# Optimization experiments

Measured on AMD Instinct MI355X. Metric: run time of the kernel, lower is better.

## Reference

```python
import jax, jax.numpy as jnp
import numpy as np

N_FEATURES = 3072
LATENT_DIM = 128
BATCH = 8192


def setup_inputs() -> dict:
    key = jax.random.key(0)
    k1, k2, k3, k4 = jax.random.split(key, 4)
    example = jax.random.normal(k1, (BATCH, N_FEATURES), dtype=jnp.float32)
    # small-ish W so C = W W^T + sigma^2 I is well conditioned
    W = jax.random.normal(k2, (N_FEATURES, LATENT_DIM), dtype=jnp.float32) * 0.05
    log_var = jax.random.normal(k3, (1,), dtype=jnp.float32) * 0.1
    training_mean = jax.random.normal(k4, (N_FEATURES,), dtype=jnp.float32)
    return {"example": example, "W": W, "log_var": log_var, "training_mean": training_mean}


def reference(example, W, log_var, training_mean):
    n = W.shape[0]
    # C = W W^T + exp(log_var) * I   -- [n, n] covariance, as in the original
    C = W @ W.T + jnp.exp(log_var[0]) * jnp.eye(n, dtype=W.dtype)
    _, logdetC = jnp.linalg.slogdet(C)
    precision = jnp.linalg.inv(C)
    res = example.reshape(-1, n) - training_mean.reshape(1, n)  # [B, n]
    # diag(res @ precision @ res^T) computed directly, avoiding the BxB matrix
    quad = jnp.einsum("bi,ij,bj->b", res, precision, res)  # [B]
    log_2pi = np.log(2.0 * np.pi).astype(np.float32)
    log_like = -0.5 * (n * log_2pi + logdetC + quad)  # [B]
    return log_like
```

## Files before the change

kernel.cpp:

```cpp
#include <hip/hip_runtime.h>
#include <hip/hip_bf16.h>

#define N_FEAT 3072
#define LATENT 128
#define LOG2PI 1.8378770664093453f
#define GB 512
#define KHALF 1536

typedef __attribute__((ext_vector_type(8))) short short8;
typedef __attribute__((ext_vector_type(4))) float f32x4;

__device__ __forceinline__ unsigned short f2bf(float x) {
  unsigned int u = __float_as_uint(x);
  u += 0x7FFFu + ((u >> 16) & 1u);
  return (unsigned short)(u >> 16);
}

#define GR_CHUNK 64
__global__ __launch_bounds__(256) void k_prep(const float* __restrict__ W,
                                              float* __restrict__ M,
                                              unsigned short* __restrict__ Wt) {
  __shared__ __align__(16) float Ws[GR_CHUNK * 128];
  int t = threadIdx.x;
  int k0 = blockIdx.x * GR_CHUNK;
  const float* src = W + (size_t)k0 * 128;
#pragma unroll
  for (int c = 0; c < 8; ++c)
    ((float4*)Ws)[t + 256 * c] = ((const float4*)src)[t + 256 * c];
  __syncthreads();
  int tr = t >> 4, tc = t & 15;
  float acc[8][8];
#pragma unroll
  for (int r = 0; r < 8; ++r)
#pragma unroll
    for (int c = 0; c < 8; ++c) acc[r][c] = 0.f;
#pragma unroll 2
  for (int k = 0; k < GR_CHUNK; ++k) {
    f32x4 a0 = *(f32x4*)&Ws[k * 128 + 8 * tr];
    f32x4 a1 = *(f32x4*)&Ws[k * 128 + 8 * tr + 4];
    f32x4 b0 = *(f32x4*)&Ws[k * 128 + 8 * tc];
    f32x4 b1 = *(f32x4*)&Ws[k * 128 + 8 * tc + 4];
    float av[8] = {a0.x, a0.y, a0.z, a0.w, a1.x, a1.y, a1.z, a1.w};
    float bv[8] = {b0.x, b0.y, b0.z, b0.w, b1.x, b1.y, b1.z, b1.w};
#pragma unroll
    for (int r = 0; r < 8; ++r)
#pragma unroll
      for (int c = 0; c < 8; ++c) acc[r][c] = fmaf(av[r], bv[c], acc[r][c]);
  }
  float* dst = M + (size_t)(8 * tr) * 128 + 8 * tc;
#pragma unroll
  for (int r = 0; r < 8; ++r)
#pragma unroll
    for (int c = 0; c < 8; ++c) atomicAdd(&dst[r * 128 + c], acc[r][c]);
  int n = t >> 1, h = t & 1;
  unsigned pk[16];
#pragma unroll
  for (int c = 0; c < 16; ++c)
    pk[c] = (unsigned)f2bf(Ws[(h * 32 + 2 * c) * 128 + n]) |
            ((unsigned)f2bf(Ws[(h * 32 + 2 * c + 1) * 128 + n]) << 16);
  uint4* wd = (uint4*)(Wt + (size_t)n * N_FEAT + k0 + h * 32);
#pragma unroll
  for (int c = 0; c < 4; ++c)
    wd[c] = make_uint4(pk[4 * c], pk[4 * c + 1], pk[4 * c + 2], pk[4 * c + 3]);
}

__global__ __launch_bounds__(512, 4) void k_gemm(
    const float* __restrict__ ex, const float* __restrict__ mean,
    const unsigned short* __restrict__ Wt, float* __restrict__ M,
    float* __restrict__ scal, const float* __restrict__ log_var,
    float* __restrict__ T, float* __restrict__ sumsq) {
  __shared__ __align__(16) unsigned short As[2][32][72];
  __shared__ __align__(16) unsigned short Bs[2][128][72];
  __shared__ float prow[2][128], pcol[2][128], dbuf[2], diag[128], red[2];
  int t = threadIdx.x;

  if (blockIdx.x == GB) {
    bool act = t < 256;
    int itr = t >> 4, itc = t & 15;
    float lv = log_var[0];
    float sig2 = expf(lv);
    float a[8][8];
    if (act) {
      const float* srcM = M + (size_t)(8 * itr) * 128 + 8 * itc;
#pragma unroll
      for (int r = 0; r < 8; ++r) {
        f32x4 v0 = *(const f32x4*)(srcM + r * 128);
        f32x4 v1 = *(const f32x4*)(srcM + r * 128 + 4);
        a[r][0] = v0.x; a[r][1] = v0.y; a[r][2] = v0.z; a[r][3] = v0.w;
        a[r][4] = v1.x; a[r][5] = v1.y; a[r][6] = v1.z; a[r][7] = v1.w;
      }
      if (itr == itc) {
#pragma unroll
        for (int r = 0; r < 8; ++r) a[r][r] += sig2;
      }
      if (itr == 0) {
#pragma unroll
        for (int c = 0; c < 8; ++c) prow[0][8 * itc + c] = a[0][c];
      }
      if (itc == 0) {
#pragma unroll
        for (int r = 0; r < 8; ++r) pcol[0][8 * itr + r] = a[r][0];
      }
      if (t == 0) dbuf[0] = a[0][0];
    }
    __syncthreads();
    for (int kb = 0; kb < 16; ++kb) {
#pragma unroll
      for (int lk = 0; lk < 8; ++lk) {
        const int k = kb * 8 + lk;
        const int buf = k & 1;
        if (act) {
          float d = dbuf[buf];
          if (t == 0) diag[k] = d;
          float p = 1.0f / d;
          float pr[8], pc[8];
#pragma unroll
          for (int c = 0; c < 8; ++c) pr[c] = prow[buf][8 * itc + c] * p;
#pragma unroll
          for (int r = 0; r < 8; ++r) pc[r] = pcol[buf][8 * itr + r];
#pragma unroll
          for (int r = 0; r < 8; ++r)
#pragma unroll
            for (int c = 0; c < 8; ++c) a[r][c] = fmaf(-pc[r], pr[c], a[r][c]);
          bool myrow = (itr == (k >> 3));
          bool mycol = (itc == (k >> 3));
          if (myrow) {
#pragma unroll
            for (int c = 0; c < 8; ++c) a[lk][c] = pr[c];
          }
          if (mycol) {
#pragma unroll
            for (int r = 0; r < 8; ++r) a[r][lk] = -p * pc[r];
          }
          if (myrow && mycol) a[lk][lk] = p;
          if (k + 1 < 128) {
            const int nb = buf ^ 1;
            const int nl = (lk + 1) & 7;
            const int nr = (k + 1) >> 3;
            if (itr == nr) {
#pragma unroll
              for (int c = 0; c < 8; ++c) prow[nb][8 * itc + c] = a[nl][c];
            }
            if (itc == nr) {
#pragma unroll
              for (int r = 0; r < 8; ++r) pcol[nb][8 * itr + r] = a[r][nl];
            }
            if (itr == nr && itc == nr) dbuf[nb] = a[nl][nl];
          }
        }
        __syncthreads();
      }
    }
    if (act) {
      float* dst = M + (size_t)(8 * itr) * 128 + 8 * itc;
#pragma unroll
      for (int r = 0; r < 8; ++r) {
        f32x4 v0 = {a[r][0], a[r][1], a[r][2], a[r][3]};
        f32x4 v1 = {a[r][4], a[r][5], a[r][6], a[r][7]};
        *(f32x4*)(dst + r * 128) = v0;
        *(f32x4*)(dst + r * 128 + 4) = v1;
      }
    }
    float ld = 0.f;
    if (t < 128) ld = logf(diag[t]);
#pragma unroll
    for (int o = 1; o < 64; o <<= 1) ld += __shfl_xor(ld, o);
    if (t == 0) red[0] = ld;
    if (t == 64) red[1] = ld;
    __syncthreads();
    if (t == 0) {
      scal[0] = -0.5f * (N_FEAT * LOG2PI + (float)(N_FEAT - LATENT) * lv +
                         (red[0] + red[1]));
      scal[1] = expf(-lv);
    }
    return;
  }

  int half = blockIdx.x >> 8;
  int r0 = (blockIdx.x & 255) * 32;
  int kbase = half * KHALF;

  int arow = t >> 4, aseg = t & 15;
  const float* ep = ex + (size_t)(r0 + arow) * N_FEAT + kbase + aseg * 4;
  const float* mp = mean + kbase + aseg * 4;
  int sA = (((aseg >> 1) + arow) & 7) * 8 + (aseg & 1) * 4;
  int brow = t >> 2, bq = t & 3;
  const unsigned short* wp = Wt + (size_t)brow * N_FEAT + kbase + bq * 16;
  int sB = ((bq + brow) & 3) * 16;

  int lane = t & 63, w = t >> 6;
  int wr = w & 1, wc = w >> 1;
  int fr = lane & 15, fq = lane >> 4;
  int ar = wr * 16 + fr;
  int cA0 = ((fq + ar) & 7) * 8;
  int cA1 = ((fq + 4 + ar) & 7) * 8;
  int n0 = wc * 32 + fr, n1 = n0 + 16;
  int c00 = (((fq >> 1) + n0) & 3) * 16 + (fq & 1) * 8;
  int c01 = (((fq >> 1) + 2 + n0) & 3) * 16 + (fq & 1) * 8;
  int c10 = (((fq >> 1) + n1) & 3) * 16 + (fq & 1) * 8;
  int c11 = (((fq >> 1) + 2 + n1) & 3) * 16 + (fq & 1) * 8;

  f32x4 acc0 = {0.f, 0.f, 0.f, 0.f}, acc1 = {0.f, 0.f, 0.f, 0.f};
  float sq = 0.f;

  float4 e = *(const float4*)ep;
  float4 m = *(const float4*)mp;
  uint4 g0 = *(const uint4*)wp;
  uint4 g1 = *(const uint4*)(wp + 8);

#pragma unroll 2
  for (int it = 0; it < 24; ++it) {
    const int buf = it & 1;
    float rx = e.x - m.x, ry = e.y - m.y, rz = e.z - m.z, rw = e.w - m.w;
    sq = fmaf(rx, rx, sq); sq = fmaf(ry, ry, sq);
    sq = fmaf(rz, rz, sq); sq = fmaf(rw, rw, sq);
    uint2 pa;
    pa.x = (unsigned)f2bf(rx) | ((unsigned)f2bf(ry) << 16);
    pa.y = (unsigned)f2bf(rz) | ((unsigned)f2bf(rw) << 16);
    *(uint2*)&As[buf][arow][sA] = pa;
    *(uint4*)&Bs[buf][brow][sB] = g0;
    *(uint4*)&Bs[buf][brow][sB + 8] = g1;
    __syncthreads();
    if (it + 1 < 24) {
      e = *(const float4*)(ep + (it + 1) * 64);
      m = *(const float4*)(mp + (it + 1) * 64);
      g0 = *(const uint4*)(wp + (it + 1) * 64);
      g1 = *(const uint4*)(wp + (it + 1) * 64 + 8);
    }
    short8 a0 = *(const short8*)&As[buf][ar][cA0];
    short8 a1 = *(const short8*)&As[buf][ar][cA1];
    short8 b00 = *(const short8*)&Bs[buf][n0][c00];
    short8 b01 = *(const short8*)&Bs[buf][n0][c01];
    short8 b10 = *(const short8*)&Bs[buf][n1][c10];
    short8 b11 = *(const short8*)&Bs[buf][n1][c11];
    acc0 = __builtin_amdgcn_mfma_f32_16x16x32_bf16(a0, b00, acc0, 0, 0, 0);
    acc0 = __builtin_amdgcn_mfma_f32_16x16x32_bf16(a1, b01, acc0, 0, 0, 0);
    acc1 = __builtin_amdgcn_mfma_f32_16x16x32_bf16(a0, b10, acc1, 0, 0, 0);
    acc1 = __builtin_amdgcn_mfma_f32_16x16x32_bf16(a1, b11, acc1, 0, 0, 0);
  }

  sq += __shfl_xor(sq, 1); sq += __shfl_xor(sq, 2);
  sq += __shfl_xor(sq, 4); sq += __shfl_xor(sq, 8);
  if (aseg == 0) atomicAdd(&sumsq[r0 + arow], sq);

  float* tp = T + (size_t)(r0 + wr * 16 + fq * 4) * 128 + wc * 32 + fr;
#pragma unroll
  for (int ii = 0; ii < 4; ++ii) {
    atomicAdd(tp + (size_t)ii * 128, acc0[ii]);
    atomicAdd(tp + (size_t)ii * 128 + 16, acc1[ii]);
  }
}

__global__ __launch_bounds__(256) void k_epi(const float* __restrict__ T,
                                             const float* __restrict__ sumsq,
                                             const float* __restrict__ Minv,
                                             const float* __restrict__ scal,
                                             float* __restrict__ out) {
  __shared__ __align__(16) float Ts[32][132];
  __shared__ float rs[32];
  int t = threadIdx.x;
  int r0 = blockIdx.x * 32;
  int sr = t >> 3, sseg = t & 7;
  const float* tp = T + (size_t)(r0 + sr) * 128 + sseg * 16;
#pragma unroll
  for (int c = 0; c < 4; ++c) {
    float4 v = *(const float4*)(tp + c * 4);
    *(f32x4*)&Ts[sr][sseg * 16 + c * 4] = (f32x4){v.x, v.y, v.z, v.w};
  }
  if (t < 32) rs[t] = sumsq[r0 + t];
  __syncthreads();

  int rp = t >> 4, cg = t & 15;
  int ra = 2 * rp, rb = ra + 1;
  int c0 = cg * 8;
  float ya[8] = {0, 0, 0, 0, 0, 0, 0, 0};
  float yb[8] = {0, 0, 0, 0, 0, 0, 0, 0};
#pragma unroll 4
  for (int j = 0; j < 128; ++j) {
    float tav = Ts[ra][j];
    float tbv = Ts[rb][j];
    float4 v0 = *(const float4*)(Minv + j * LATENT + c0);
    float4 v1 = *(const float4*)(Minv + j * LATENT + c0 + 4);
    ya[0] = fmaf(tav, v0.x, ya[0]); ya[1] = fmaf(tav, v0.y, ya[1]);
    ya[2] = fmaf(tav, v0.z, ya[2]); ya[3] = fmaf(tav, v0.w, ya[3]);
    ya[4] = fmaf(tav, v1.x, ya[4]); ya[5] = fmaf(tav, v1.y, ya[5]);
    ya[6] = fmaf(tav, v1.z, ya[6]); ya[7] = fmaf(tav, v1.w, ya[7]);
    yb[0] = fmaf(tbv, v0.x, yb[0]); yb[1] = fmaf(tbv, v0.y, yb[1]);
    yb[2] = fmaf(tbv, v0.z, yb[2]); yb[3] = fmaf(tbv, v0.w, yb[3]);
    yb[4] = fmaf(tbv, v1.x, yb[4]); yb[5] = fmaf(tbv, v1.y, yb[5]);
    yb[6] = fmaf(tbv, v1.z, yb[6]); yb[7] = fmaf(tbv, v1.w, yb[7]);
  }
  float q0 = 0.f, q1 = 0.f;
#pragma unroll
  for (int c = 0; c < 8; ++c) {
    q0 = fmaf(ya[c], Ts[ra][c0 + c], q0);
    q1 = fmaf(yb[c], Ts[rb][c0 + c], q1);
  }
  q0 += __shfl_xor(q0, 1); q0 += __shfl_xor(q0, 2);
  q0 += __shfl_xor(q0, 4); q0 += __shfl_xor(q0, 8);
  q1 += __shfl_xor(q1, 1); q1 += __shfl_xor(q1, 2);
  q1 += __shfl_xor(q1, 4); q1 += __shfl_xor(q1, 8);
  if (cg == 0) {
    float cc = scal[0], is2 = scal[1];
    out[r0 + ra] = cc - 0.5f * is2 * (rs[ra] - q0);
    out[r0 + rb] = cc - 0.5f * is2 * (rs[rb] - q1);
  }
}

extern "C" void kernel_launch(void* const* d_in, const int* in_sizes, int n_in,
                              void* d_out, int out_size, void* d_ws, size_t ws_size,
                              hipStream_t stream) {
  (void)in_sizes; (void)n_in; (void)out_size; (void)ws_size;
  const float* ex   = (const float*)d_in[0];
  const float* W    = (const float*)d_in[1];
  const float* lv   = (const float*)d_in[2];
  const float* mean = (const float*)d_in[3];
  float* out = (float*)d_out;

  float* M = (float*)d_ws;
  float* scal = M + 16384;
  float* T = scal + 64;
  float* sumsq = T + 1048576;
  unsigned short* Wt = (unsigned short*)(sumsq + 8192);

  hipMemsetAsync(M, 0, (size_t)(16384 + 64 + 1048576 + 8192) * sizeof(float),
                 stream);
  k_prep<<<48, 256, 0, stream>>>(W, M, Wt);
  k_gemm<<<GB + 1, 512, 0, stream>>>(ex, mean, Wt, M, scal, lv, T, sumsq);
  k_epi<<<256, 256, 0, stream>>>(T, sumsq, M, scal, out);
}
```

Measured before the change: 265.5 us.

## Drop split-K atomics and memset; use 16-row full-K GEMM blocks and partial-sum Gram reduce

The GEMM no longer splits K across two block halves that accumulate into T and sumsq with atomics. Each block now covers 16 rows over the full K with 256 threads and plain stores. The W^T W Gram partials are written to a per-block scratch area and summed by a new small reduce kernel, which removes the atomics and the large workspace memset. The factorization block moves to block 0 with all 256 threads active. The LDS swizzle and the order of prefetch and stores change to one barrier per iteration, at the cost of one extra kernel launch and a longer serial K loop per block.

```diff
diff --git a/kernel.cpp b/kernel.cpp
--- a/kernel.cpp
+++ b/kernel.cpp
@@ -4,8 +4,7 @@
 #define N_FEAT 3072
 #define LATENT 128
 #define LOG2PI 1.8378770664093453f
-#define GB 512
-#define KHALF 1536
+#define NGB 512
 
 typedef __attribute__((ext_vector_type(8))) short short8;
 typedef __attribute__((ext_vector_type(4))) float f32x4;
@@ -18,7 +17,7 @@
 
 #define GR_CHUNK 64
 __global__ __launch_bounds__(256) void k_prep(const float* __restrict__ W,
-                                              float* __restrict__ M,
+                                              float* __restrict__ Mp,
                                               unsigned short* __restrict__ Wt) {
   __shared__ __align__(16) float Ws[GR_CHUNK * 128];
   int t = threadIdx.x;
@@ -47,11 +46,12 @@
 #pragma unroll
       for (int c = 0; c < 8; ++c) acc[r][c] = fmaf(av[r], bv[c], acc[r][c]);
   }
-  float* dst = M + (size_t)(8 * tr) * 128 + 8 * tc;
-#pragma unroll
-  for (int r = 0; r < 8; ++r)
-#pragma unroll
-    for (int c = 0; c < 8; ++c) atomicAdd(&dst[r * 128 + c], acc[r][c]);
+  float* dst = Mp + (size_t)blockIdx.x * 16384 + (size_t)(8 * tr) * 128 + 8 * tc;
+#pragma unroll
+  for (int r = 0; r < 8; ++r) {
+    *(f32x4*)(dst + r * 128) = (f32x4){acc[r][0], acc[r][1], acc[r][2], acc[r][3]};
+    *(f32x4*)(dst + r * 128 + 4) = (f32x4){acc[r][4], acc[r][5], acc[r][6], acc[r][7]};
+  }
   int n = t >> 1, h = t & 1;
   unsigned pk[16];
 #pragma unroll
@@ -64,23 +64,31 @@
     wd[c] = make_uint4(pk[4 * c], pk[4 * c + 1], pk[4 * c + 2], pk[4 * c + 3]);
 }
 
-__global__ __launch_bounds__(512, 4) void k_gemm(
+__global__ __launch_bounds__(256) void k_red(const float* __restrict__ Mp,
+                                             float* __restrict__ M) {
+  int i = blockIdx.x * 256 + threadIdx.x;
+  float s = 0.f;
+#pragma unroll
+  for (int p = 0; p < 48; ++p) s += Mp[(size_t)p * 16384 + i];
+  M[i] = s;
+}
+
+__global__ __launch_bounds__(256, 4) void k_gemm(
     const float* __restrict__ ex, const float* __restrict__ mean,
     const unsigned short* __restrict__ Wt, float* __restrict__ M,
     float* __restrict__ scal, const float* __restrict__ log_var,
     float* __restrict__ T, float* __restrict__ sumsq) {
-  __shared__ __align__(16) unsigned short As[2][32][72];
-  __shared__ __align__(16) unsigned short Bs[2][128][72];
+  __shared__ __align__(16) unsigned short As[2][16][64];
+  __shared__ __align__(16) unsigned short Bs[2][128][64];
   __shared__ float prow[2][128], pcol[2][128], dbuf[2], diag[128], red[2];
   int t = threadIdx.x;
 
-  if (blockIdx.x == GB) {
-    bool act = t < 256;
+  if (blockIdx.x == 0) {
     int itr = t >> 4, itc = t & 15;
     float lv = log_var[0];
     float sig2 = expf(lv);
     float a[8][8];
-    if (act) {
+    {
       const float* srcM = M + (size_t)(8 * itr) * 128 + 8 * itc;
 #pragma unroll
       for (int r = 0; r < 8; ++r) {
@@ -109,7 +117,7 @@
       for (int lk = 0; lk < 8; ++lk) {
         const int k = kb * 8 + lk;
         const int buf = k & 1;
-        if (act) {
+        {
           float d = dbuf[buf];
           if (t == 0) diag[k] = d;
           float p = 1.0f / d;
@@ -151,7 +159,7 @@
         __syncthreads();
       }
     }
-    if (act) {
+    {
       float* dst = M + (size_t)(8 * itr) * 128 + 8 * itc;
 #pragma unroll
       for (int r = 0; r < 8; ++r) {
@@ -176,78 +184,95 @@
     return;
   }
 
-  int half = blockIdx.x >> 8;
-  int r0 = (blockIdx.x & 255) * 32;
-  int kbase = half * KHALF;
-
-  int arow = t >> 4, aseg = t & 15;
-  const float* ep = ex + (size_t)(r0 + arow) * N_FEAT + kbase + aseg * 4;
-  const float* mp = mean + kbase + aseg * 4;
-  int sA = (((aseg >> 1) + arow) & 7) * 8 + (aseg & 1) * 4;
-  int brow = t >> 2, bq = t & 3;
-  const unsigned short* wp = Wt + (size_t)brow * N_FEAT + kbase + bq * 16;
-  int sB = ((bq + brow) & 3) * 16;
+  int r0 = (blockIdx.x - 1) * 16;
+
+  int arow = t >> 4, ag = t & 15;
+  const float* ep = ex + (size_t)(r0 + arow) * N_FEAT + ag * 4;
+  const float* mp = mean + ag * 4;
+  int awoff = arow * 128 + ((((ag >> 1) + arow) & 7) << 4) + (ag & 1) * 8;
+
+  int brow = t >> 1, bh = t & 1;
+  const unsigned short* wp = Wt + (size_t)brow * N_FEAT + bh * 32;
+  int bwoff[4];
+#pragma unroll
+  for (int j = 0; j < 4; ++j)
+    bwoff[j] = brow * 128 + ((((bh * 4 + j) + brow) & 7) << 4);
 
   int lane = t & 63, w = t >> 6;
-  int wr = w & 1, wc = w >> 1;
   int fr = lane & 15, fq = lane >> 4;
-  int ar = wr * 16 + fr;
-  int cA0 = ((fq + ar) & 7) * 8;
-  int cA1 = ((fq + 4 + ar) & 7) * 8;
-  int n0 = wc * 32 + fr, n1 = n0 + 16;
-  int c00 = (((fq >> 1) + n0) & 3) * 16 + (fq & 1) * 8;
-  int c01 = (((fq >> 1) + 2 + n0) & 3) * 16 + (fq & 1) * 8;
-  int c10 = (((fq >> 1) + n1) & 3) * 16 + (fq & 1) * 8;
-  int c11 = (((fq >> 1) + 2 + n1) & 3) * 16 + (fq & 1) * 8;
+  int n0 = w * 32 + fr, n1 = n0 + 16;
+  int aoff[2], boff0[2], boff1[2];
+#pragma unroll
+  for (int kk = 0; kk < 2; ++kk) {
+    int s = kk * 4 + fq;
+    aoff[kk]  = fr * 128 + (((s + fr) & 7) << 4);
+    boff0[kk] = n0 * 128 + (((s + n0) & 7) << 4);
+    boff1[kk] = n1 * 128 + (((s + n1) & 7) << 4);
+  }
 
   f32x4 acc0 = {0.f, 0.f, 0.f, 0.f}, acc1 = {0.f, 0.f, 0.f, 0.f};
   float sq = 0.f;
-
-  float4 e = *(const float4*)ep;
-  float4 m = *(const float4*)mp;
-  uint4 g0 = *(const uint4*)wp;
-  uint4 g1 = *(const uint4*)(wp + 8);
-
-#pragma unroll 2
-  for (int it = 0; it < 24; ++it) {
-    const int buf = it & 1;
+  float4 e, m;
+  uint4 g[4];
+
+  auto pack_a = [&](char* dstA) {
     float rx = e.x - m.x, ry = e.y - m.y, rz = e.z - m.z, rw = e.w - m.w;
     sq = fmaf(rx, rx, sq); sq = fmaf(ry, ry, sq);
     sq = fmaf(rz, rz, sq); sq = fmaf(rw, rw, sq);
     uint2 pa;
     pa.x = (unsigned)f2bf(rx) | ((unsigned)f2bf(ry) << 16);
     pa.y = (unsigned)f2bf(rz) | ((unsigned)f2bf(rw) << 16);
-    *(uint2*)&As[buf][arow][sA] = pa;
-    *(uint4*)&Bs[buf][brow][sB] = g0;
-    *(uint4*)&Bs[buf][brow][sB + 8] = g1;
-    __syncthreads();
-    if (it + 1 < 24) {
+    *(uint2*)(dstA + awoff) = pa;
+  };
+  auto write_b = [&](char* dstB) {
+#pragma unroll
+    for (int j = 0; j < 4; ++j) *(uint4*)(dstB + bwoff[j]) = g[j];
+  };
+
+  e = *(const float4*)ep;
+  m = *(const float4*)mp;
+#pragma unroll
+  for (int j = 0; j < 4; ++j) g[j] = *(const uint4*)(wp + j * 8);
+  pack_a((char*)As);
+  write_b((char*)Bs);
+  __syncthreads();
+
+#pragma unroll 2
+  for (int it = 0; it < 48; ++it) {
+    const int buf = it & 1;
+    if (it + 1 < 48) {
       e = *(const float4*)(ep + (it + 1) * 64);
       m = *(const float4*)(mp + (it + 1) * 64);
-      g0 = *(const uint4*)(wp + (it + 1) * 64);
-      g1 = *(const uint4*)(wp + (it + 1) * 64 + 8);
-    }
-    short8 a0 = *(const short8*)&As[buf][ar][cA0];
-    short8 a1 = *(const short8*)&As[buf][ar][cA1];
-    short8 b00 = *(const short8*)&Bs[buf][n0][c00];
-    short8 b01 = *(const short8*)&Bs[buf][n0][c01];
-    short8 b10 = *(const short8*)&Bs[buf][n1][c10];
-    short8 b11 = *(const short8*)&Bs[buf][n1][c11];
-    acc0 = __builtin_amdgcn_mfma_f32_16x16x32_bf16(a0, b00, acc0, 0, 0, 0);
-    acc0 = __builtin_amdgcn_mfma_f32_16x16x32_bf16(a1, b01, acc0, 0, 0, 0);
-    acc1 = __builtin_amdgcn_mfma_f32_16x16x32_bf16(a0, b10, acc1, 0, 0, 0);
-    acc1 = __builtin_amdgcn_mfma_f32_16x16x32_bf16(a1, b11, acc1, 0, 0, 0);
+      const unsigned short* wq = wp + (it + 1) * 64;
+#pragma unroll
+      for (int j = 0; j < 4; ++j) g[j] = *(const uint4*)(wq + j * 8);
+    }
+    char* Ar = (char*)As + buf * 2048;
+    char* Br = (char*)Bs + buf * 16384;
+#pragma unroll
+    for (int kk = 0; kk < 2; ++kk) {
+      short8 a  = *(const short8*)(Ar + aoff[kk]);
+      short8 b0 = *(const short8*)(Br + boff0[kk]);
+      short8 b1 = *(const short8*)(Br + boff1[kk]);
+      acc0 = __builtin_amdgcn_mfma_f32_16x16x32_bf16(a, b0, acc0, 0, 0, 0);
+      acc1 = __builtin_amdgcn_mfma_f32_16x16x32_bf16(a, b1, acc1, 0, 0, 0);
+    }
+    if (it + 1 < 48) {
+      pack_a((char*)As + (buf ^ 1) * 2048);
+      write_b((char*)Bs + (buf ^ 1) * 16384);
+    }
+    __syncthreads();
   }
 
   sq += __shfl_xor(sq, 1); sq += __shfl_xor(sq, 2);
   sq += __shfl_xor(sq, 4); sq += __shfl_xor(sq, 8);
-  if (aseg == 0) atomicAdd(&sumsq[r0 + arow], sq);
-
-  float* tp = T + (size_t)(r0 + wr * 16 + fq * 4) * 128 + wc * 32 + fr;
+  if (ag == 0) sumsq[r0 + arow] = sq;
+
+  float* tp = T + (size_t)(r0 + fq * 4) * 128 + w * 32 + fr;
 #pragma unroll
   for (int ii = 0; ii < 4; ++ii) {
-    atomicAdd(tp + (size_t)ii * 128, acc0[ii]);
-    atomicAdd(tp + (size_t)ii * 128 + 16, acc1[ii]);
+    tp[(size_t)ii * 128] = acc0[ii];
+    tp[(size_t)ii * 128 + 16] = acc1[ii];
   }
 }
 
@@ -322,10 +347,10 @@
   float* T = scal + 64;
   float* sumsq = T + 1048576;
   unsigned short* Wt = (unsigned short*)(sumsq + 8192);
-
-  hipMemsetAsync(M, 0, (size_t)(16384 + 64 + 1048576 + 8192) * sizeof(float),
-                 stream);
-  k_prep<<<48, 256, 0, stream>>>(W, M, Wt);
-  k_gemm<<<GB + 1, 512, 0, stream>>>(ex, mean, Wt, M, scal, lv, T, sumsq);
+  float* Mp = T;
+
+  k_prep<<<48, 256, 0, stream>>>(W, Mp, Wt);
+  k_red<<<64, 256, 0, stream>>>(Mp, M);
+  k_gemm<<<NGB + 1, 256, 0, stream>>>(ex, mean, Wt, M, scal, lv, T, sumsq);
   k_epi<<<256, 256, 0, stream>>>(T, sumsq, M, scal, out);
 }
```

After: 393.9 us. 1.48x slower.
